# Kernel tuning notes

Measured on AMD Instinct MI355X. Metric: run time of the kernel, lower is better.

The kernel has to match this reference:

```python
import jax, jax.numpy as jnp
import numpy as np

B, T, DIN = 4, 1024, 512
DLIN, DK, DV, NH = 1024, 1024, 1024, 16

def setup_inputs() -> dict:
    key = jax.random.key(0)
    ks = jax.random.split(key, 5)
    s = 0.02
    return {
        "data": jax.random.normal(ks[0], (B, T, DIN), dtype=jnp.float32),
        "W_in": jax.random.normal(ks[1], (DLIN, DIN + T), dtype=jnp.float32) * s,
        "W_q": jax.random.normal(ks[2], (DK, DLIN), dtype=jnp.float32) * s,
        "W_k": jax.random.normal(ks[3], (DK, DLIN), dtype=jnp.float32) * s,
        "W_v": jax.random.normal(ks[4], (DV, DLIN), dtype=jnp.float32) * s,
    }

def reference(data, W_in, W_q, W_k, W_v):
    b, t, d_in = data.shape
    nh = NH
    dk = DK // nh
    dv = DV // nh
    scale = 1.0 / np.sqrt(dk).astype(np.float32)
    # concat identity positional one-hots: [B, T, DIN + T]
    p = jnp.broadcast_to(jnp.eye(t, dtype=data.dtype), (b, t, t))
    x = jnp.concatenate([data, p], axis=-1)
    h = jnp.einsum('btc,dc->btd', x, W_in)            # [B,T,DLIN]
    q = jnp.einsum('btd,kd->btk', h, W_q).reshape(b, t, nh, dk).transpose(0, 2, 1, 3)
    k = jnp.einsum('btd,kd->btk', h, W_k).reshape(b, t, nh, dk).transpose(0, 2, 1, 3)
    v = jnp.einsum('btd,kd->btk', h, W_v).reshape(b, t, nh, dv).transpose(0, 2, 1, 3)
    dist = jnp.einsum('bhqd,bhkd->bhqk', q, k) * scale   # [B,H,T,T]
    dist = jax.nn.softmax(dist, axis=-1)
    att = jnp.einsum('bhqk,bhkd->bhqd', dist, v)         # [B,H,T,dv]
    return att.transpose(0, 2, 1, 3).reshape(b, t, DV)
```

## Files before the change

### kernel.cpp

```cpp
#include <hip/hip_runtime.h>
#include <stdint.h>


typedef __bf16 bf16x8 __attribute__((ext_vector_type(8)));
typedef float f32x4 __attribute__((ext_vector_type(4)));
typedef unsigned short u16;
typedef u16 u16x8 __attribute__((ext_vector_type(8)));

#define MFMA16(a, b, c) __builtin_amdgcn_mfma_f32_16x16x32_bf16(a, b, c, 0, 0, 0)

using gld_src_t = const __attribute__((address_space(1))) unsigned int*;
using gld_dst_t = __attribute__((address_space(3))) unsigned int*;

__device__ __forceinline__ u16 f2bf(float f) {
  uint32_t u = __builtin_bit_cast(uint32_t, f);
  uint32_t r = (u + 0x7fffu + ((u >> 16) & 1u)) >> 16;
  return (u16)r;
}


__global__ __launch_bounds__(256) void cvt_all(
    const float* __restrict__ data, const float* __restrict__ wq,
    const float* __restrict__ wk, const float* __restrict__ wv,
    u16* __restrict__ o_data, u16* __restrict__ o_wq,
    u16* __restrict__ o_wk, u16* __restrict__ o_wv) {
  const float* s;
  u16* o;
  int n;
  switch (blockIdx.y) {
    case 0: s = data; o = o_data; n = 4096 * 512; break;
    case 1: s = wq; o = o_wq; n = 1024 * 1024; break;
    case 2: s = wk; o = o_wk; n = 1024 * 1024; break;
    default: s = wv; o = o_wv; n = 1024 * 1024; break;
  }
  int i = (blockIdx.x * 256 + threadIdx.x) * 8;
  if (i >= n) return;
  float4 a = *(const float4*)(s + i);
  float4 b = *(const float4*)(s + i + 4);
  u16x8 v;
  v[0] = f2bf(a.x); v[1] = f2bf(a.y); v[2] = f2bf(a.z); v[3] = f2bf(a.w);
  v[4] = f2bf(b.x); v[5] = f2bf(b.y); v[6] = f2bf(b.z); v[7] = f2bf(b.w);
  *(u16x8*)(o + i) = v;
}

__global__ __launch_bounds__(256) void cvt_win(const float* __restrict__ Win,
                                               u16* __restrict__ wd) {
  int i = (blockIdx.x * 256 + threadIdx.x) * 8;
  if (i >= 1024 * 512) return;
  int row = i >> 9, col = i & 511;
  const float* s = Win + (size_t)row * 1536 + col;
  float4 a = *(const float4*)s;
  float4 b = *(const float4*)(s + 4);
  u16x8 v;
  v[0] = f2bf(a.x); v[1] = f2bf(a.y); v[2] = f2bf(a.z); v[3] = f2bf(a.w);
  v[4] = f2bf(b.x); v[5] = f2bf(b.y); v[6] = f2bf(b.z); v[7] = f2bf(b.w);
  *(u16x8*)(wd + i) = v;
}


template <int EPI>
__global__ __launch_bounds__(256) void gemm_bt(
    const u16* __restrict__ A, const u16* __restrict__ B0,
    const u16* __restrict__ B1, const u16* __restrict__ B2,
    const float* __restrict__ Wpos, u16* __restrict__ O0,
    u16* __restrict__ O1, u16* __restrict__ O2, int K) {
  __shared__ u16 Ash[128 * 64];
  __shared__ u16 Bsh[128 * 64];
  const int tid = threadIdx.x;
  const int lane = tid & 63;
  const int w = tid >> 6;
  const int wr = w >> 1, wc = w & 1;
  const int m0 = blockIdx.x * 128, n0 = blockIdx.y * 128;

  const u16* Bw;
  u16* Out;
  if constexpr (EPI == 0) {
    Bw = B0; Out = O0;
  } else {
    int z = blockIdx.z;
    Bw = (z == 0) ? B0 : (z == 1) ? B1 : B2;
    Out = (z == 0) ? O0 : (z == 1) ? O1 : O2;
  }

  f32x4 acc[4][4];
#pragma unroll
  for (int m = 0; m < 4; ++m)
#pragma unroll
    for (int n = 0; n < 4; ++n) acc[m][n] = (f32x4){0.f, 0.f, 0.f, 0.f};

  for (int kt = 0; kt < K; kt += 64) {
    __syncthreads();
#pragma unroll
    for (int i = 0; i < 4; ++i) {
      int c = i * 256 + tid;
      int row = c >> 3;
      int sg = (c & 7) ^ (row & 7);
      const u16* srcA = A + (size_t)(m0 + row) * K + kt + sg * 8;
      __builtin_amdgcn_global_load_lds((gld_src_t)srcA,
                                       (gld_dst_t)&Ash[(i * 256 + w * 64) * 8],
                                       16, 0, 0);
      const u16* srcB = Bw + (size_t)(n0 + row) * K + kt + sg * 8;
      __builtin_amdgcn_global_load_lds((gld_src_t)srcB,
                                       (gld_dst_t)&Bsh[(i * 256 + w * 64) * 8],
                                       16, 0, 0);
    }
    __syncthreads();
#pragma unroll
    for (int kk = 0; kk < 2; ++kk) {
      bf16x8 af[4], bfr[4];
#pragma unroll
      for (int m = 0; m < 4; ++m) {
        int r = wr * 64 + m * 16 + (lane & 15);
        int slot = (kk * 4 + (lane >> 4)) ^ (r & 7);
        af[m] = *(const bf16x8*)((const char*)Ash + r * 128 + slot * 16);
      }
#pragma unroll
      for (int n = 0; n < 4; ++n) {
        int r = wc * 64 + n * 16 + (lane & 15);
        int slot = (kk * 4 + (lane >> 4)) ^ (r & 7);
        bfr[n] = *(const bf16x8*)((const char*)Bsh + r * 128 + slot * 16);
      }
#pragma unroll
      for (int m = 0; m < 4; ++m)
#pragma unroll
        for (int n = 0; n < 4; ++n) acc[m][n] = MFMA16(af[m], bfr[n], acc[m][n]);
    }
  }

#pragma unroll
  for (int m = 0; m < 4; ++m) {
#pragma unroll
    for (int n = 0; n < 4; ++n) {
      int r0 = m0 + wr * 64 + m * 16 + ((lane >> 4) << 2);
      int col = n0 + wc * 64 + n * 16 + (lane & 15);
      if constexpr (EPI == 0) {
        int t0 = r0 & 1023;
        float4 pb = *(const float4*)(Wpos + (size_t)col * 1536 + 512 + t0);
        float pbv[4] = {pb.x, pb.y, pb.z, pb.w};
#pragma unroll
        for (int q = 0; q < 4; ++q)
          Out[(size_t)(r0 + q) * 1024 + col] = f2bf(acc[m][n][q] + pbv[q]);
      } else {
        int hd = col >> 6, j = col & 63;
        int b = r0 >> 10;
        size_t bh = (size_t)(b * 16 + hd) * 65536;
#pragma unroll
        for (int q = 0; q < 4; ++q) {
          int t = (r0 + q) & 1023;
          size_t idx = (blockIdx.z == 2) ? bh + (size_t)j * 1024 + t
                                         : bh + (size_t)t * 64 + j;
          Out[idx] = f2bf(acc[m][n][q]);
        }
      }
    }
  }
}

__global__ __launch_bounds__(256) void attn(const u16* __restrict__ Q,
                                            const u16* __restrict__ Kt,
                                            const u16* __restrict__ Vt,
                                            float* __restrict__ out) {
  __shared__ u16 Ksh[64 * 64];
  __shared__ u16 Vsh[64 * 64];
  __shared__ u16 Psh[4][16 * 72];
  const int tid = threadIdx.x, lane = tid & 63, w = tid >> 6;
  const int bh = blockIdx.y, q0 = blockIdx.x * 64;
  const size_t base = (size_t)bh * 65536;

  bf16x8 qf[2];
  {
    int r = q0 + w * 16 + (lane & 15);
    const u16* qp = Q + base + (size_t)r * 64 + (lane >> 4) * 8;
    qf[0] = *(const bf16x8*)qp;
    qf[1] = *(const bf16x8*)(qp + 32);
  }

  f32x4 o[4];
#pragma unroll
  for (int n = 0; n < 4; ++n) o[n] = (f32x4){0.f, 0.f, 0.f, 0.f};
  float lsum[4] = {0.f, 0.f, 0.f, 0.f};

  for (int kv0 = 0; kv0 < 1024; kv0 += 64) {
    __syncthreads();
#pragma unroll
    for (int i = 0; i < 2; ++i) {
      int c = i * 256 + tid;
      int row = c >> 3, sp = c & 7;
      int spx = sp ^ (row & 7);
      bf16x8 kd = *(const bf16x8*)(Kt + base + (size_t)(kv0 + row) * 64 + sp * 8);
      *(bf16x8*)((char*)Ksh + row * 128 + spx * 16) = kd;
      bf16x8 vd = *(const bf16x8*)(Vt + base + (size_t)row * 1024 + kv0 + sp * 8);
      *(bf16x8*)((char*)Vsh + row * 128 + spx * 16) = vd;
    }
    __syncthreads();

    f32x4 s[4];
#pragma unroll
    for (int n = 0; n < 4; ++n) s[n] = (f32x4){0.f, 0.f, 0.f, 0.f};
#pragma unroll
    for (int n = 0; n < 4; ++n) {
#pragma unroll
      for (int kk = 0; kk < 2; ++kk) {
        int r = n * 16 + (lane & 15);
        int slot = (kk * 4 + (lane >> 4)) ^ (r & 7);
        bf16x8 kf = *(const bf16x8*)((const char*)Ksh + r * 128 + slot * 16);
        s[n] = MFMA16(qf[kk], kf, s[n]);
      }
    }

    float rs[4] = {0.f, 0.f, 0.f, 0.f};
    u16* pp = (u16*)Psh[w];
#pragma unroll
    for (int n = 0; n < 4; ++n) {
#pragma unroll
      for (int q = 0; q < 4; ++q) {
        float p = __expf(s[n][q] * 0.125f);
        rs[q] += p;
        int row = ((lane >> 4) << 2) + q;
        pp[row * 72 + n * 16 + (lane & 15)] = f2bf(p);
      }
    }
#pragma unroll
    for (int off = 1; off < 16; off <<= 1)
#pragma unroll
      for (int q = 0; q < 4; ++q) rs[q] += __shfl_xor(rs[q], off, 64);
#pragma unroll
    for (int q = 0; q < 4; ++q) lsum[q] += rs[q];

    bf16x8 pf[2];
#pragma unroll
    for (int kk = 0; kk < 2; ++kk)
      pf[kk] = *(const bf16x8*)(pp + (lane & 15) * 72 + kk * 32 + (lane >> 4) * 8);
#pragma unroll
    for (int n = 0; n < 4; ++n) {
#pragma unroll
      for (int kk = 0; kk < 2; ++kk) {
        int r = n * 16 + (lane & 15);
        int slot = (kk * 4 + (lane >> 4)) ^ (r & 7);
        bf16x8 vf = *(const bf16x8*)((const char*)Vsh + r * 128 + slot * 16);
        o[n] = MFMA16(pf[kk], vf, o[n]);
      }
    }
  }

  const int b = bh >> 4, hd = bh & 15;
#pragma unroll
  for (int n = 0; n < 4; ++n) {
#pragma unroll
    for (int q = 0; q < 4; ++q) {
      int t = q0 + w * 16 + ((lane >> 4) << 2) + q;
      int j = n * 16 + (lane & 15);
      out[((size_t)(b * 1024 + t)) * 1024 + hd * 64 + j] = o[n][q] / lsum[q];
    }
  }
}


extern "C" void kernel_launch(void* const* d_in, const int* in_sizes, int n_in,
                              void* d_out, int out_size, void* d_ws,
                              size_t ws_size, hipStream_t stream) {
  const float* data = (const float*)d_in[0];
  const float* Win = (const float*)d_in[1];
  const float* Wq = (const float*)d_in[2];
  const float* Wk = (const float*)d_in[3];
  const float* Wv = (const float*)d_in[4];
  float* out = (float*)d_out;

  char* ws = (char*)d_ws;
  u16* data_b = (u16*)ws; ws += (size_t)4096 * 512 * 2;
  u16* wd_b = (u16*)ws;   ws += (size_t)1024 * 512 * 2;
  u16* wq_b = (u16*)ws;   ws += (size_t)1024 * 1024 * 2;
  u16* wk_b = (u16*)ws;   ws += (size_t)1024 * 1024 * 2;
  u16* wv_b = (u16*)ws;   ws += (size_t)1024 * 1024 * 2;
  u16* h_b = (u16*)ws;    ws += (size_t)4096 * 1024 * 2;
  u16* q_b = (u16*)ws;    ws += (size_t)4194304 * 2;
  u16* k_b = (u16*)ws;    ws += (size_t)4194304 * 2;
  u16* vt_b = (u16*)ws;   ws += (size_t)4194304 * 2;

  cvt_all<<<dim3(1024, 4), 256, 0, stream>>>(data, Wq, Wk, Wv, data_b, wq_b,
                                             wk_b, wv_b);
  cvt_win<<<dim3(256), 256, 0, stream>>>(Win, wd_b);
  gemm_bt<0><<<dim3(32, 8, 1), 256, 0, stream>>>(data_b, wd_b, wd_b, wd_b, Win,
                                                 h_b, h_b, h_b, 512);
  gemm_bt<1><<<dim3(32, 8, 3), 256, 0, stream>>>(h_b, wq_b, wk_b, wv_b, nullptr,
                                                 q_b, k_b, vt_b, 1024);
  attn<<<dim3(16, 64), 256, 0, stream>>>(q_b, k_b, vt_b, out);
}
```

Before: 182.7 us.

## Rewrite attention with 32x32 MFMA, register-resident P, and folded exp2 scale

The attention kernel is restructured so each wave computes S transposed with 32x32x16 MFMAs, reading K and V directly from global memory (L2) instead of staging them in LDS, and feeding P straight from registers into the PV MFMA. The softmax scale times log2(e) is folded into the Q projection epilogue so exp2 can be used directly. Output is staged through LDS for coalesced float4 stores, and blocks are remapped so head/batch pairs interleave. The intent is to remove per-tile syncthreads, the LDS round-trip for P, and the per-element scale multiply, at the risk of higher global/L2 traffic from uncached K/V loads and no max subtraction, which could overflow for large logits.

```diff
diff --git a/kernel.cpp b/kernel.cpp
--- a/kernel.cpp
+++ b/kernel.cpp
@@ -3,11 +3,14 @@
 
 
 typedef __bf16 bf16x8 __attribute__((ext_vector_type(8)));
+typedef __bf16 bf16x4v __attribute__((ext_vector_type(4)));
 typedef float f32x4 __attribute__((ext_vector_type(4)));
+typedef float f32x16 __attribute__((ext_vector_type(16)));
 typedef unsigned short u16;
 typedef u16 u16x8 __attribute__((ext_vector_type(8)));
 
 #define MFMA16(a, b, c) __builtin_amdgcn_mfma_f32_16x16x32_bf16(a, b, c, 0, 0, 0)
+#define MFMA32(a, b, c) __builtin_amdgcn_mfma_f32_32x32x16_bf16(a, b, c, 0, 0, 0)
 
 using gld_src_t = const __attribute__((address_space(1))) unsigned int*;
 using gld_dst_t = __attribute__((address_space(3))) unsigned int*;
@@ -141,6 +144,7 @@
         for (int q = 0; q < 4; ++q)
           Out[(size_t)(r0 + q) * 1024 + col] = f2bf(acc[m][n][q] + pbv[q]);
       } else {
+        float qsc = (blockIdx.z == 0) ? 0.18033688011112042f : 1.0f;
         int hd = col >> 6, j = col & 63;
         int b = r0 >> 10;
         size_t bh = (size_t)(b * 16 + hd) * 65536;
@@ -149,109 +153,104 @@
           int t = (r0 + q) & 1023;
           size_t idx = (blockIdx.z == 2) ? bh + (size_t)j * 1024 + t
                                          : bh + (size_t)t * 64 + j;
-          Out[idx] = f2bf(acc[m][n][q]);
+          Out[idx] = f2bf(acc[m][n][q] * qsc);
         }
       }
     }
   }
 }
 
-__global__ __launch_bounds__(256) void attn(const u16* __restrict__ Q,
-                                            const u16* __restrict__ Kt,
-                                            const u16* __restrict__ Vt,
-                                            float* __restrict__ out) {
-  __shared__ u16 Ksh[64 * 64];
-  __shared__ u16 Vsh[64 * 64];
-  __shared__ u16 Psh[4][16 * 72];
+__global__ __launch_bounds__(256, 2) void attn(const u16* __restrict__ Q,
+                                               const u16* __restrict__ K,
+                                               const u16* __restrict__ Vt,
+                                               float* __restrict__ out) {
+  __shared__ float lbuf[4][32 * 66];
   const int tid = threadIdx.x, lane = tid & 63, w = tid >> 6;
-  const int bh = blockIdx.y, q0 = blockIdx.x * 64;
+  const int q = lane & 31, hi = lane >> 5;
+  const int flat = blockIdx.x;
+  const int bh = (flat & 7) * 8 + ((flat >> 3) & 7);
+  const int q0 = (flat >> 6) * 128 + w * 32;
   const size_t base = (size_t)bh * 65536;
 
-  bf16x8 qf[2];
-  {
-    int r = q0 + w * 16 + (lane & 15);
-    const u16* qp = Q + base + (size_t)r * 64 + (lane >> 4) * 8;
-    qf[0] = *(const bf16x8*)qp;
-    qf[1] = *(const bf16x8*)(qp + 32);
-  }
-
-  f32x4 o[4];
-#pragma unroll
-  for (int n = 0; n < 4; ++n) o[n] = (f32x4){0.f, 0.f, 0.f, 0.f};
-  float lsum[4] = {0.f, 0.f, 0.f, 0.f};
-
-  for (int kv0 = 0; kv0 < 1024; kv0 += 64) {
-    __syncthreads();
-#pragma unroll
-    for (int i = 0; i < 2; ++i) {
-      int c = i * 256 + tid;
-      int row = c >> 3, sp = c & 7;
-      int spx = sp ^ (row & 7);
-      bf16x8 kd = *(const bf16x8*)(Kt + base + (size_t)(kv0 + row) * 64 + sp * 8);
-      *(bf16x8*)((char*)Ksh + row * 128 + spx * 16) = kd;
-      bf16x8 vd = *(const bf16x8*)(Vt + base + (size_t)row * 1024 + kv0 + sp * 8);
-      *(bf16x8*)((char*)Vsh + row * 128 + spx * 16) = vd;
-    }
-    __syncthreads();
-
-    f32x4 s[4];
-#pragma unroll
-    for (int n = 0; n < 4; ++n) s[n] = (f32x4){0.f, 0.f, 0.f, 0.f};
-#pragma unroll
-    for (int n = 0; n < 4; ++n) {
-#pragma unroll
-      for (int kk = 0; kk < 2; ++kk) {
-        int r = n * 16 + (lane & 15);
-        int slot = (kk * 4 + (lane >> 4)) ^ (r & 7);
-        bf16x8 kf = *(const bf16x8*)((const char*)Ksh + r * 128 + slot * 16);
-        s[n] = MFMA16(qf[kk], kf, s[n]);
-      }
-    }
-
-    float rs[4] = {0.f, 0.f, 0.f, 0.f};
-    u16* pp = (u16*)Psh[w];
-#pragma unroll
-    for (int n = 0; n < 4; ++n) {
-#pragma unroll
-      for (int q = 0; q < 4; ++q) {
-        float p = __expf(s[n][q] * 0.125f);
-        rs[q] += p;
-        int row = ((lane >> 4) << 2) + q;
-        pp[row * 72 + n * 16 + (lane & 15)] = f2bf(p);
-      }
-    }
-#pragma unroll
-    for (int off = 1; off < 16; off <<= 1)
-#pragma unroll
-      for (int q = 0; q < 4; ++q) rs[q] += __shfl_xor(rs[q], off, 64);
-#pragma unroll
-    for (int q = 0; q < 4; ++q) lsum[q] += rs[q];
-
-    bf16x8 pf[2];
-#pragma unroll
-    for (int kk = 0; kk < 2; ++kk)
-      pf[kk] = *(const bf16x8*)(pp + (lane & 15) * 72 + kk * 32 + (lane >> 4) * 8);
-#pragma unroll
-    for (int n = 0; n < 4; ++n) {
-#pragma unroll
-      for (int kk = 0; kk < 2; ++kk) {
-        int r = n * 16 + (lane & 15);
-        int slot = (kk * 4 + (lane >> 4)) ^ (r & 7);
-        bf16x8 vf = *(const bf16x8*)((const char*)Vsh + r * 128 + slot * 16);
-        o[n] = MFMA16(pf[kk], vf, o[n]);
-      }
-    }
-  }
-
+  bf16x8 qf[4];
+#pragma unroll
+  for (int ks = 0; ks < 4; ++ks)
+    qf[ks] = *(const bf16x8*)(Q + base + (size_t)(q0 + q) * 64 + ks * 16 + hi * 8);
+
+  f32x16 ot[2];
+#pragma unroll
+  for (int r = 0; r < 16; ++r) {
+    ot[0][r] = 0.f;
+    ot[1][r] = 0.f;
+  }
+  float lsum = 0.f;
+
+  const u16* Kp = K + base + (size_t)q * 64 + hi * 8;
+  const u16* Vp = Vt + base + (size_t)q * 1024 + hi * 4;
+
+  for (int kv0 = 0; kv0 < 1024; kv0 += 32) {
+    f32x16 st;
+#pragma unroll
+    for (int r = 0; r < 16; ++r) st[r] = 0.f;
+#pragma unroll
+    for (int ks = 0; ks < 4; ++ks) {
+      bf16x8 kf = *(const bf16x8*)(Kp + (size_t)kv0 * 64 + ks * 16);
+      st = MFMA32(kf, qf[ks], st);
+    }
+    float pe[16];
+#pragma unroll
+    for (int r = 0; r < 16; ++r) pe[r] = __builtin_exp2f(st[r]);
+    {
+      float t0 = (pe[0] + pe[1]) + (pe[2] + pe[3]);
+      float t1 = (pe[4] + pe[5]) + (pe[6] + pe[7]);
+      float t2 = (pe[8] + pe[9]) + (pe[10] + pe[11]);
+      float t3 = (pe[12] + pe[13]) + (pe[14] + pe[15]);
+      lsum += (t0 + t1) + (t2 + t3);
+    }
+#pragma unroll
+    for (int s = 0; s < 2; ++s) {
+      bf16x8 pf;
+#pragma unroll
+      for (int j = 0; j < 8; ++j) pf[j] = (__bf16)pe[8 * s + j];
+#pragma unroll
+      for (int d = 0; d < 2; ++d) {
+        const u16* vr = Vp + (size_t)(32 * d) * 1024 + kv0 + 16 * s;
+        bf16x4v v0 = *(const bf16x4v*)vr;
+        bf16x4v v1 = *(const bf16x4v*)(vr + 8);
+        bf16x8 vf;
+#pragma unroll
+        for (int j = 0; j < 4; ++j) {
+          vf[j] = v0[j];
+          vf[4 + j] = v1[j];
+        }
+        ot[d] = MFMA32(vf, pf, ot[d]);
+      }
+    }
+  }
+
+  lsum += __shfl_xor(lsum, 32, 64);
+  float ri = 1.0f / lsum;
+
+  float* lb = &lbuf[w][0];
+#pragma unroll
+  for (int d = 0; d < 2; ++d)
+#pragma unroll
+    for (int rr = 0; rr < 16; rr += 2) {
+      int dv = 32 * d + (rr & 3) + 8 * (rr >> 2) + 4 * hi;
+      *(float2*)(lb + q * 66 + dv) =
+          make_float2(ot[d][rr] * ri, ot[d][rr + 1] * ri);
+    }
+  __syncthreads();
   const int b = bh >> 4, hd = bh & 15;
 #pragma unroll
-  for (int n = 0; n < 4; ++n) {
-#pragma unroll
-    for (int q = 0; q < 4; ++q) {
-      int t = q0 + w * 16 + ((lane >> 4) << 2) + q;
-      int j = n * 16 + (lane & 15);
-      out[((size_t)(b * 1024 + t)) * 1024 + hd * 64 + j] = o[n][q] / lsum[q];
-    }
+  for (int i = 0; i < 8; ++i) {
+    int row = i * 4 + (lane >> 4);
+    const float* lr = lb + row * 66 + (lane & 15) * 4;
+    float2 x0 = *(const float2*)lr;
+    float2 x1 = *(const float2*)(lr + 2);
+    float4 v = make_float4(x0.x, x0.y, x1.x, x1.y);
+    *(float4*)(out + ((size_t)(b * 1024 + q0 + row)) * 1024 + hd * 64 +
+               (lane & 15) * 4) = v;
   }
 }
 
@@ -284,5 +283,5 @@
                                                  h_b, h_b, h_b, 512);
   gemm_bt<1><<<dim3(32, 8, 3), 256, 0, stream>>>(h_b, wq_b, wk_b, wv_b, nullptr,
                                                  q_b, k_b, vt_b, 1024);
-  attn<<<dim3(16, 64), 256, 0, stream>>>(q_b, k_b, vt_b, out);
-}
+  attn<<<dim3(512), 256, 0, stream>>>(q_b, k_b, vt_b, out);
+}
```

After: 217.0 us. +18.8%, slower.
